# Performance work log

Hardware: AMD Instinct MI355X
Metric: run time of the kernel (lower is better)

## Reference

```python
import jax, jax.numpy as jnp
import numpy as np

B, N, D, K = 16, 65536, 24, 512
ATTRACTION_WEIGHT = 1.0
REPULSION_WEIGHT = 1.5
MARGIN_WEIGHT = 5.0
THRESHOLD = 0.5
MARGIN = 0.2
TAU = 0.7


def setup_inputs() -> dict:
    key = jax.random.key(0)
    k1, k2, k3 = jax.random.split(key, 3)
    beta = jax.random.normal(k1, (B, N, 1), jnp.float32)
    embed = jax.random.normal(k2, (B, N, D), jnp.float32)
    # First K hits of each event are the condensation points (one per instance),
    # remaining hits get a random instance id in [0, K).
    rand_sid = jax.random.randint(k3, (B, N - K), 0, K, jnp.int32)
    cp_sid = jnp.broadcast_to(jnp.arange(K, dtype=jnp.int32), (B, K))
    slice_id = jnp.concatenate([cp_sid, rand_sid], axis=1)
    is_cp = jnp.concatenate(
        [jnp.ones((B, K), jnp.int32), jnp.zeros((B, N - K), jnp.int32)], axis=1)
    return {"beta": beta, "embed": embed, "slice_id": slice_id, "is_cp": is_cp}


def _per_batch(beta_b, emb_b, sid, cp):
    # beta_b: [N], emb_b: [N, D], sid: [N] int, cp: [N] int
    n = beta_b.shape[0]
    f32 = beta_b.dtype
    cp_mask = cp == 1
    pos_count = cp_mask.sum()
    neg_count = n - pos_count

    seg_cnt = jax.ops.segment_sum(jnp.ones((n,), f32), sid, num_segments=K)
    inst_present = seg_cnt > 0
    cp_per_inst = jax.ops.segment_sum(cp_mask.astype(f32), sid, num_segments=K)
    valid_inst = inst_present & (cp_per_inst == 1)  # inst_cp.sum() == 1

    # --- grouped softmax CE over each instance (temperature TAU) ---
    logits = jnp.clip(beta_b, -20.0, 20.0) / TAU
    seg_max = jax.ops.segment_max(logits, sid, num_segments=K)
    safe_max = jnp.where(inst_present, seg_max, 0.0)
    ex = jnp.exp(logits - safe_max[sid])
    denom = jax.ops.segment_sum(ex, sid, num_segments=K)
    cp_logit = jax.ops.segment_sum(jnp.where(cp_mask, logits, 0.0), sid,
                                   num_segments=K)  # exactly one cp when valid
    p_cp = jnp.exp(cp_logit - safe_max) / jnp.maximum(denom, 1e-30)
    loss_inst = -jnp.log(p_cp + 1e-9)
    slice_count = valid_inst.sum()
    beta_slice_ce = jnp.where(valid_inst, loss_inst, 0.0).sum() / jnp.maximum(slice_count, 1)

    # --- margin loss on sigmoid(beta) ---
    beta_prob = jax.nn.sigmoid(jnp.clip(beta_b, -20.0, 20.0))
    pos_m = jnp.where(cp_mask, jax.nn.relu(THRESHOLD + MARGIN - beta_prob), 0.0).sum() \
        / jnp.maximum(pos_count, 1)
    neg_m = jnp.where(cp_mask, 0.0, jax.nn.relu(beta_prob - (THRESHOLD - MARGIN))).sum() \
        / jnp.maximum(neg_count, 1)
    beta_loss = beta_slice_ce + MARGIN_WEIGHT * (pos_m + neg_m)

    # --- attraction: hits pulled to first CP of their instance ---
    idx = jnp.arange(n, dtype=jnp.int32)
    first_cp = jax.ops.segment_min(jnp.where(cp_mask, idx, n), sid, num_segments=K)
    has_cp = (first_cp < n) & inst_present
    cp_emb = emb_b[jnp.minimum(first_cp, n - 1)]  # [K, D]
    d2 = jnp.minimum(((emb_b - cp_emb[sid]) ** 2).sum(-1), 50.0)
    d2_mean = jax.ops.segment_sum(d2, sid, num_segments=K) / jnp.maximum(seg_cnt, 1.0)
    attraction = ATTRACTION_WEIGHT * jnp.where(has_cp, d2_mean, 0.0).sum()

    # --- repulsion: pairwise exp(-d2) between CP embeddings (incl. diagonal) ---
    m = has_cp.astype(f32)
    mcount = m.sum()
    sq = (cp_emb ** 2).sum(-1)
    pd2 = sq[:, None] + sq[None, :] - 2.0 * (cp_emb @ cp_emb.T)
    pd2 = jnp.clip(pd2, 0.0, 50.0)
    rep = (jnp.exp(-pd2) * (m[:, None] * m[None, :])).sum() / jnp.maximum(mcount * mcount, 1.0)
    repulsion = jnp.where(mcount > 1, REPULSION_WEIGHT * rep, 0.0)

    valid = (pos_count >= 1) & (neg_count >= 1) & (slice_count > 0)
    total = beta_loss + attraction + repulsion
    return total, beta_loss, attraction, repulsion, valid


def reference(beta, embed, slice_id, is_cp):
    beta = jnp.nan_to_num(jnp.squeeze(beta, -1), nan=0.0, posinf=0.0, neginf=0.0)
    embed = jnp.nan_to_num(embed, nan=0.0, posinf=0.0, neginf=0.0)
    total, bl, al, rl, valid = jax.vmap(_per_batch)(beta, embed, slice_id, is_cp)
    v = valid.astype(beta.dtype)
    count = v.sum()
    safe = jnp.maximum(count, 1.0)
    ok = count > 0
    final = jnp.where(ok, (total * v).sum() / safe, 0.0)
    beta_log = jnp.where(ok, (bl * v).sum() / safe, 0.0)
    attr_log = jnp.where(ok, (al * v).sum() / safe, 0.0)
    repl_log = jnp.where(ok, (rl * v).sum() / safe, 0.0)
    return final, beta_log, attr_log, repl_log
```

## Files before the change

### kernel.cpp

```cpp
#include <hip/hip_runtime.h>
#include <math.h>

#define BB 16
#define NN 65536
#define DD 24
#define KK 512
#define CH 64
#define HPB (NN / CH)
#define TPB 256
#define RPB 8

__device__ __forceinline__ float fixnum(float v) {
  return __builtin_isfinite(v) ? v : 0.0f;
}

__device__ __forceinline__ float blockReduceSum(float v, float* sbuf) {
  __syncthreads();
  #pragma unroll
  for (int off = 32; off > 0; off >>= 1) v += __shfl_down(v, off, 64);
  int wid = threadIdx.x >> 6, lane = threadIdx.x & 63;
  if (lane == 0) sbuf[wid] = v;
  __syncthreads();
  return sbuf[0] + sbuf[1] + sbuf[2] + sbuf[3];
}

__global__ __launch_bounds__(TPB) void k1_seg(
    const float* __restrict__ beta, const int* __restrict__ sid,
    const int* __restrict__ iscp,
    float* __restrict__ cnt_p, float* __restrict__ den_p,
    float* __restrict__ cpc_p, float* __restrict__ cpl_p,
    int* __restrict__ first_p, float* __restrict__ marg_p)
{
  __shared__ float s_cnt[KK], s_den[KK], s_cpc[KK], s_cpl[KK];
  __shared__ int   s_first[KK];
  __shared__ float sred[4];
  int b = blockIdx.x >> 6, c = blockIdx.x & 63, t = threadIdx.x;
  for (int k = t; k < KK; k += TPB) {
    s_cnt[k] = 0.f; s_den[k] = 0.f; s_cpc[k] = 0.f; s_cpl[k] = 0.f; s_first[k] = NN;
  }
  __syncthreads();
  int h0 = c * HPB + t * 4;
  size_t g0 = (size_t)b * NN + h0;
  float4 bv = *(const float4*)(beta + g0);
  int4   sv = *(const int4*)(sid + g0);
  int4   cv = *(const int4*)(iscp + g0);
  float pm = 0.f, nm = 0.f;
  float bs[4] = {bv.x, bv.y, bv.z, bv.w};
  int   ss[4] = {sv.x, sv.y, sv.z, sv.w};
  int   cs[4] = {cv.x, cv.y, cv.z, cv.w};
  #pragma unroll
  for (int j = 0; j < 4; ++j) {
    float bc = fminf(fmaxf(fixnum(bs[j]), -20.f), 20.f);
    float logit = bc * (1.0f / 0.7f);
    int s = ss[j];
    atomicAdd(&s_cnt[s], 1.0f);
    atomicAdd(&s_den[s], __expf(logit));
    float prob = 1.0f / (1.0f + __expf(-bc));
    if (cs[j] == 1) {
      atomicAdd(&s_cpc[s], 1.0f);
      atomicAdd(&s_cpl[s], logit);
      atomicMin(&s_first[s], h0 + j);
      pm += fmaxf(0.7f - prob, 0.f);
    } else {
      nm += fmaxf(prob - 0.3f, 0.f);
    }
  }
  float pms = blockReduceSum(pm, sred);
  float nms = blockReduceSum(nm, sred);
  if (t == 0) { marg_p[2 * blockIdx.x] = pms; marg_p[2 * blockIdx.x + 1] = nms; }
  __syncthreads();
  size_t base = ((size_t)b * CH + c) * KK;
  for (int k = t; k < KK; k += TPB) {
    cnt_p[base + k] = s_cnt[k]; den_p[base + k] = s_den[k];
    cpc_p[base + k] = s_cpc[k]; cpl_p[base + k] = s_cpl[k];
    first_p[base + k] = s_first[k];
  }
}

__global__ __launch_bounds__(TPB) void k2_fin(
    const float* __restrict__ embed,
    const float* __restrict__ cnt_p, const float* __restrict__ den_p,
    const float* __restrict__ cpc_p, const float* __restrict__ cpl_p,
    const int* __restrict__ first_p,
    float* __restrict__ seg_cnt, float* __restrict__ loss_v,
    float* __restrict__ valid_f, float* __restrict__ has_cp_f,
    float* __restrict__ cpc_tot, float* __restrict__ cp_emb,
    float* __restrict__ d2_acc, float* __restrict__ rep_acc)
{
  int idx = blockIdx.x * TPB + threadIdx.x;
  int b = idx >> 9, k = idx & (KK - 1);
  float cnt = 0.f, den = 0.f, cpc = 0.f, cpl = 0.f;
  int fc = NN;
  #pragma unroll 8
  for (int c = 0; c < CH; ++c) {
    size_t base = ((size_t)b * CH + c) * KK + k;
    cnt += cnt_p[base]; den += den_p[base];
    cpc += cpc_p[base]; cpl += cpl_p[base];
    fc = min(fc, first_p[base]);
  }
  bool present = cnt > 0.f;
  bool vinst = present && (cpc == 1.0f);
  float p = __expf(cpl) / fmaxf(den, 1e-30f);
  seg_cnt[idx] = cnt;
  cpc_tot[idx] = cpc;
  loss_v[idx] = vinst ? -__logf(p + 1e-9f) : 0.f;
  valid_f[idx] = vinst ? 1.f : 0.f;
  has_cp_f[idx] = ((fc < NN) && present) ? 1.f : 0.f;
  d2_acc[idx] = 0.f;
  if (idx < BB) rep_acc[idx] = 0.f;
  int row = fc < NN ? fc : NN - 1;
  const float4* src = (const float4*)(embed + ((size_t)b * NN + row) * DD);
  float4* dst = (float4*)(cp_emb + (size_t)idx * DD);
  #pragma unroll
  for (int q = 0; q < DD / 4; ++q) {
    float4 v = src[q];
    v.x = fixnum(v.x); v.y = fixnum(v.y); v.z = fixnum(v.z); v.w = fixnum(v.w);
    dst[q] = v;
  }
}

__global__ __launch_bounds__(TPB) void k3_attr_rep(
    const float* __restrict__ embed, const int* __restrict__ sid,
    const float* __restrict__ cp_emb, const float* __restrict__ has_cp_f,
    float* __restrict__ d2_acc, float* __restrict__ rep_acc)
{
  __shared__ __align__(16) float s_ce[KK * DD];
  __shared__ float s_tile[64 * 25];
  __shared__ float s_d2[KK];
  int b = blockIdx.x >> 6, c = blockIdx.x & 63, t = threadIdx.x;

  const float4* ceg = (const float4*)(cp_emb + (size_t)b * KK * DD);
  float4* ces = (float4*)s_ce;
  #pragma unroll
  for (int i = 0; i < (KK * DD / 4) / TPB; ++i)
    ces[t + i * TPB] = ceg[t + i * TPB];
  for (int k = t; k < KK; k += TPB) s_d2[k] = 0.f;

  int hl = t >> 2, q = t & 3, d0 = q * 6;
  int rbase = hl * 25 + d0;
  int wI[3];
  #pragma unroll
  for (int j = 0; j < 3; ++j) {
    int f = 2 * (t + j * TPB);
    int h = f / 24;
    wI[j] = h * 25 + (f - h * 24);
  }

  size_t hit0 = (size_t)b * NN + (size_t)c * HPB;
  const float2* eb2 = (const float2*)(embed + hit0 * DD);
  const int* sidb = sid + hit0;

  float2 r[3];
  #pragma unroll
  for (int j = 0; j < 3; ++j) r[j] = eb2[t + j * TPB];
  __syncthreads();

  for (int tile = 0; tile < 16; ++tile) {
    #pragma unroll
    for (int j = 0; j < 3; ++j) {
      s_tile[wI[j]]     = fixnum(r[j].x);
      s_tile[wI[j] + 1] = fixnum(r[j].y);
    }
    __syncthreads();
    if (tile < 15) {
      const float2* nb = eb2 + (size_t)(tile + 1) * (64 * DD / 2);
      #pragma unroll
      for (int j = 0; j < 3; ++j) r[j] = nb[t + j * TPB];
    }
    int s = sidb[tile * 64 + hl];
    int cbase = s * DD + d0;
    float d2 = 0.f;
    #pragma unroll
    for (int d = 0; d < 6; ++d) {
      float x = s_tile[rbase + d] - s_ce[cbase + d];
      d2 += x * x;
    }
    d2 += __shfl_xor(d2, 1, 64);
    d2 += __shfl_xor(d2, 2, 64);
    if (q == 0) atomicAdd(&s_d2[s], fminf(d2, 50.f));
    __syncthreads();
  }

  for (int k = t; k < KK; k += TPB)
    atomicAdd(&d2_acc[b * KK + k], s_d2[k]);

  int j0 = t, j1 = t + TPB;
  float cj0[DD], cj1[DD];
  const float4* cj0p = (const float4*)(s_ce + j0 * DD);
  const float4* cj1p = (const float4*)(s_ce + j1 * DD);
  #pragma unroll
  for (int qq = 0; qq < DD / 4; ++qq) {
    float4 a = cj0p[qq], bq = cj1p[qq];
    cj0[qq*4] = a.x; cj0[qq*4+1] = a.y; cj0[qq*4+2] = a.z; cj0[qq*4+3] = a.w;
    cj1[qq*4] = bq.x; cj1[qq*4+1] = bq.y; cj1[qq*4+2] = bq.z; cj1[qq*4+3] = bq.w;
  }
  float m0 = has_cp_f[b * KK + j0], m1 = has_cp_f[b * KK + j1];
  float acc = 0.f;
  #pragma unroll
  for (int ri = 0; ri < RPB; ++ri) {
    int i = c * RPB + ri;
    float mi = has_cp_f[b * KK + i];
    float d20 = 0.f, d21 = 0.f;
    #pragma unroll
    for (int d = 0; d < DD; ++d) {
      float ci = s_ce[i * DD + d];
      float x0 = ci - cj0[d]; d20 += x0 * x0;
      float x1 = ci - cj1[d]; d21 += x1 * x1;
    }
    acc += mi * (m0 * __expf(-fminf(d20, 50.f)) + m1 * __expf(-fminf(d21, 50.f)));
  }
  float tot = blockReduceSum(acc, s_d2);
  if (t == 0) atomicAdd(&rep_acc[b], tot);
}

__global__ __launch_bounds__(1024) void k4_final(
    const float* __restrict__ d2_acc, const float* __restrict__ seg_cnt,
    const float* __restrict__ loss_v, const float* __restrict__ valid_f,
    const float* __restrict__ cpc_tot, const float* __restrict__ has_cp_f,
    const float* __restrict__ marg_p, const float* __restrict__ rep_acc,
    float* __restrict__ out)
{
  __shared__ float s_b[BB][5];
  int w = threadIdx.x >> 6, l = threadIdx.x & 63;
  int b = w;
  float attr = 0.f, ce = 0.f, vcnt = 0.f, pcnt = 0.f, mcnt = 0.f;
  #pragma unroll
  for (int k = l; k < KK; k += 64) {
    int idx = b * KK + k;
    float hc = has_cp_f[idx];
    attr += hc * (d2_acc[idx] / fmaxf(seg_cnt[idx], 1.f));
    ce   += loss_v[idx];
    vcnt += valid_f[idx];
    pcnt += cpc_tot[idx];
    mcnt += hc;
  }
  float pm = marg_p[(b * CH + l) * 2];
  float nm = marg_p[(b * CH + l) * 2 + 1];
  #pragma unroll
  for (int off = 32; off > 0; off >>= 1) {
    attr += __shfl_down(attr, off, 64);
    ce   += __shfl_down(ce, off, 64);
    vcnt += __shfl_down(vcnt, off, 64);
    pcnt += __shfl_down(pcnt, off, 64);
    mcnt += __shfl_down(mcnt, off, 64);
    pm   += __shfl_down(pm, off, 64);
    nm   += __shfl_down(nm, off, 64);
  }
  if (l == 0) {
    float pos = pcnt, neg = (float)NN - pos;
    float slice_ce = ce / fmaxf(vcnt, 1.f);
    float beta_loss = slice_ce + 5.0f * (pm / fmaxf(pos, 1.f) + nm / fmaxf(neg, 1.f));
    float rep = rep_acc[b] / fmaxf(mcnt * mcnt, 1.f);
    float repulsion = (mcnt > 1.f) ? 1.5f * rep : 0.f;
    float v = (pos >= 1.f && neg >= 1.f && vcnt > 0.f) ? 1.f : 0.f;
    s_b[w][0] = (beta_loss + attr + repulsion) * v;
    s_b[w][1] = beta_loss * v;
    s_b[w][2] = attr * v;
    s_b[w][3] = repulsion * v;
    s_b[w][4] = v;
  }
  __syncthreads();
  if (threadIdx.x == 0) {
    float s0 = 0.f, s1 = 0.f, s2 = 0.f, s3 = 0.f, cv = 0.f;
    #pragma unroll
    for (int i = 0; i < BB; ++i) {
      s0 += s_b[i][0]; s1 += s_b[i][1]; s2 += s_b[i][2]; s3 += s_b[i][3]; cv += s_b[i][4];
    }
    float safe = fmaxf(cv, 1.f);
    bool ok = cv > 0.f;
    out[0] = ok ? s0 / safe : 0.f;
    out[1] = ok ? s1 / safe : 0.f;
    out[2] = ok ? s2 / safe : 0.f;
    out[3] = ok ? s3 / safe : 0.f;
  }
}

extern "C" void kernel_launch(void* const* d_in, const int* in_sizes, int n_in,
                              void* d_out, int out_size, void* d_ws, size_t ws_size,
                              hipStream_t stream) {
  (void)in_sizes; (void)n_in; (void)out_size; (void)ws_size;
  const float* beta  = (const float*)d_in[0];
  const float* embed = (const float*)d_in[1];
  const int*   sid   = (const int*)d_in[2];
  const int*   iscp  = (const int*)d_in[3];
  float* out = (float*)d_out;
  char* ws = (char*)d_ws;

  size_t off = 0;
  auto alloc = [&](size_t bytes) {
    size_t o = off; off += (bytes + 255) & ~(size_t)255; return o;
  };
  const size_t BCK = (size_t)BB * CH * KK * 4;
  const size_t BKf = (size_t)BB * KK * 4;
  size_t o_cnt_p  = alloc(BCK);
  size_t o_den_p  = alloc(BCK);
  size_t o_cpc_p  = alloc(BCK);
  size_t o_cpl_p  = alloc(BCK);
  size_t o_first  = alloc(BCK);
  size_t o_marg   = alloc((size_t)BB * CH * 2 * 4);
  size_t o_segc   = alloc(BKf);
  size_t o_lossv  = alloc(BKf);
  size_t o_validf = alloc(BKf);
  size_t o_hascp  = alloc(BKf);
  size_t o_cpct   = alloc(BKf);
  size_t o_d2     = alloc(BKf);
  size_t o_cpe    = alloc((size_t)BB * KK * DD * 4);
  size_t o_rep    = alloc((size_t)BB * 4);

  k1_seg<<<BB * CH, TPB, 0, stream>>>(beta, sid, iscp,
      (float*)(ws + o_cnt_p), (float*)(ws + o_den_p),
      (float*)(ws + o_cpc_p), (float*)(ws + o_cpl_p),
      (int*)(ws + o_first), (float*)(ws + o_marg));

  k2_fin<<<(BB * KK) / TPB, TPB, 0, stream>>>(embed,
      (const float*)(ws + o_cnt_p), (const float*)(ws + o_den_p),
      (const float*)(ws + o_cpc_p), (const float*)(ws + o_cpl_p),
      (const int*)(ws + o_first),
      (float*)(ws + o_segc), (float*)(ws + o_lossv), (float*)(ws + o_validf),
      (float*)(ws + o_hascp), (float*)(ws + o_cpct), (float*)(ws + o_cpe),
      (float*)(ws + o_d2), (float*)(ws + o_rep));

  k3_attr_rep<<<BB * CH, TPB, 0, stream>>>(embed, sid,
      (const float*)(ws + o_cpe), (const float*)(ws + o_hascp),
      (float*)(ws + o_d2), (float*)(ws + o_rep));

  k4_final<<<1, 1024, 0, stream>>>((const float*)(ws + o_d2),
      (const float*)(ws + o_segc), (const float*)(ws + o_lossv),
      (const float*)(ws + o_validf), (const float*)(ws + o_cpct),
      (const float*)(ws + o_hascp), (const float*)(ws + o_marg),
      (const float*)(ws + o_rep), out);
}
```

Baseline: 206.1 us.

## Fuse four kernels into one cooperative persistent kernel with grid syncs

Replaces the four-launch pipeline with a single cooperative kernel of 256 blocks × 512 threads that runs segment reduction, per-instance finalize, attraction/repulsion and the final reduction, separated by grid.sync(). It also changes the work split: 16 chunks per batch instead of 64, each block handling twice as many hits per tile, and 32 repulsion rows per block. The aim is to remove launch gaps and inter-kernel tail effects. In exchange it uses fewer, larger blocks, relies on grid-wide barriers, and runs the finalize stage on only 16 blocks, with the old path kept as a fallback if the cooperative launch fails.

```diff
diff --git a/kernel.cpp b/kernel.cpp
--- a/kernel.cpp
+++ b/kernel.cpp
@@ -1,10 +1,17 @@
 #include <hip/hip_runtime.h>
+#include <hip/hip_cooperative_groups.h>
 #include <math.h>
+
+namespace cg = cooperative_groups;
 
 #define BB 16
 #define NN 65536
 #define DD 24
 #define KK 512
+#define FBLK 256
+#define FTPB 512
+#define FCPB 16
+#define FHPB (NN / FCPB)
 #define CH 64
 #define HPB (NN / CH)
 #define TPB 256
@@ -14,14 +21,274 @@
   return __builtin_isfinite(v) ? v : 0.0f;
 }
 
-__device__ __forceinline__ float blockReduceSum(float v, float* sbuf) {
+__device__ __forceinline__ float blockReduceSum8(float v, float* sbuf) {
   __syncthreads();
   #pragma unroll
   for (int off = 32; off > 0; off >>= 1) v += __shfl_down(v, off, 64);
   int wid = threadIdx.x >> 6, lane = threadIdx.x & 63;
   if (lane == 0) sbuf[wid] = v;
   __syncthreads();
+  float s = 0.f;
+  #pragma unroll
+  for (int i = 0; i < 8; ++i) s += sbuf[i];
+  return s;
+}
+
+__device__ __forceinline__ float blockReduceSum(float v, float* sbuf) {
+  __syncthreads();
+  #pragma unroll
+  for (int off = 32; off > 0; off >>= 1) v += __shfl_down(v, off, 64);
+  int wid = threadIdx.x >> 6, lane = threadIdx.x & 63;
+  if (lane == 0) sbuf[wid] = v;
+  __syncthreads();
   return sbuf[0] + sbuf[1] + sbuf[2] + sbuf[3];
+}
+
+__global__ __launch_bounds__(FTPB, 2) void kfused(
+    const float* __restrict__ beta, const float* __restrict__ embed,
+    const int* __restrict__ sid, const int* __restrict__ iscp,
+    float* __restrict__ cnt_p, float* __restrict__ den_p,
+    float* __restrict__ cpc_p, float* __restrict__ cpl_p,
+    int* __restrict__ first_p, float* __restrict__ marg_p,
+    float* __restrict__ seg_cnt, float* __restrict__ loss_v,
+    float* __restrict__ valid_f, float* __restrict__ has_cp_f,
+    float* __restrict__ cpc_tot, float* __restrict__ cp_emb,
+    float* __restrict__ d2_acc, float* __restrict__ rep_acc,
+    float* __restrict__ out)
+{
+  __shared__ __align__(16) float s_ce[KK * DD];
+  __shared__ float s_tile[128 * 25];
+  __shared__ float s_d2[KK];
+  __shared__ float sred[8];
+  __shared__ float s_b[BB][5];
+
+  cg::grid_group grid = cg::this_grid();
+  int blk = blockIdx.x, t = threadIdx.x;
+  int b = blk >> 4, qc = blk & 15;
+
+  {
+    float* s_cnt = s_ce;
+    float* s_den = s_ce + KK;
+    float* s_cpc = s_ce + 2 * KK;
+    float* s_cpl = s_ce + 3 * KK;
+    int*   s_first = (int*)(s_ce + 4 * KK);
+    if (t < KK) {
+      s_cnt[t] = 0.f; s_den[t] = 0.f; s_cpc[t] = 0.f; s_cpl[t] = 0.f;
+      s_first[t] = NN;
+    }
+    __syncthreads();
+    int h0 = qc * FHPB + t * 8;
+    size_t g0 = (size_t)b * NN + h0;
+    float4 bv0 = *(const float4*)(beta + g0);
+    float4 bv1 = *(const float4*)(beta + g0 + 4);
+    int4   sv0 = *(const int4*)(sid + g0);
+    int4   sv1 = *(const int4*)(sid + g0 + 4);
+    int4   cv0 = *(const int4*)(iscp + g0);
+    int4   cv1 = *(const int4*)(iscp + g0 + 4);
+    float bs[8] = {bv0.x, bv0.y, bv0.z, bv0.w, bv1.x, bv1.y, bv1.z, bv1.w};
+    int   ss[8] = {sv0.x, sv0.y, sv0.z, sv0.w, sv1.x, sv1.y, sv1.z, sv1.w};
+    int   cs[8] = {cv0.x, cv0.y, cv0.z, cv0.w, cv1.x, cv1.y, cv1.z, cv1.w};
+    float pm = 0.f, nm = 0.f;
+    #pragma unroll
+    for (int j = 0; j < 8; ++j) {
+      float bc = fminf(fmaxf(fixnum(bs[j]), -20.f), 20.f);
+      float logit = bc * (1.0f / 0.7f);
+      int s = ss[j];
+      atomicAdd(&s_cnt[s], 1.0f);
+      atomicAdd(&s_den[s], __expf(logit));
+      float prob = 1.0f / (1.0f + __expf(-bc));
+      if (cs[j] == 1) {
+        atomicAdd(&s_cpc[s], 1.0f);
+        atomicAdd(&s_cpl[s], logit);
+        atomicMin(&s_first[s], h0 + j);
+        pm += fmaxf(0.7f - prob, 0.f);
+      } else {
+        nm += fmaxf(prob - 0.3f, 0.f);
+      }
+    }
+    float pms = blockReduceSum8(pm, sred);
+    float nms = blockReduceSum8(nm, sred);
+    if (t == 0) { marg_p[2 * blk] = pms; marg_p[2 * blk + 1] = nms; }
+    __syncthreads();
+    size_t base = (size_t)blk * KK;
+    if (t < KK) {
+      cnt_p[base + t] = s_cnt[t]; den_p[base + t] = s_den[t];
+      cpc_p[base + t] = s_cpc[t]; cpl_p[base + t] = s_cpl[t];
+      first_p[base + t] = s_first[t];
+    }
+  }
+  grid.sync();
+
+  if (blk < BB) {
+    int bb = blk, k = t;
+    float cnt = 0.f, den = 0.f, cpc = 0.f, cpl = 0.f;
+    int fc = NN;
+    #pragma unroll 4
+    for (int c = 0; c < FCPB; ++c) {
+      size_t base = ((size_t)bb * FCPB + c) * KK + k;
+      cnt += cnt_p[base]; den += den_p[base];
+      cpc += cpc_p[base]; cpl += cpl_p[base];
+      fc = min(fc, first_p[base]);
+    }
+    int idx = bb * KK + k;
+    bool present = cnt > 0.f;
+    bool vinst = present && (cpc == 1.0f);
+    float p = __expf(cpl) / fmaxf(den, 1e-30f);
+    seg_cnt[idx] = cnt;
+    cpc_tot[idx] = cpc;
+    loss_v[idx] = vinst ? -__logf(p + 1e-9f) : 0.f;
+    valid_f[idx] = vinst ? 1.f : 0.f;
+    has_cp_f[idx] = ((fc < NN) && present) ? 1.f : 0.f;
+    d2_acc[idx] = 0.f;
+    if (blk == 0 && t < BB) rep_acc[t] = 0.f;
+    int row = fc < NN ? fc : NN - 1;
+    const float4* src = (const float4*)(embed + ((size_t)bb * NN + row) * DD);
+    float4* dst = (float4*)(cp_emb + (size_t)idx * DD);
+    #pragma unroll
+    for (int q = 0; q < DD / 4; ++q) {
+      float4 v = src[q];
+      v.x = fixnum(v.x); v.y = fixnum(v.y); v.z = fixnum(v.z); v.w = fixnum(v.w);
+      dst[q] = v;
+    }
+  }
+  grid.sync();
+
+  {
+    const float4* ceg = (const float4*)(cp_emb + (size_t)b * KK * DD);
+    float4* ces = (float4*)s_ce;
+    #pragma unroll
+    for (int i = 0; i < (KK * DD / 4) / FTPB; ++i)
+      ces[t + i * FTPB] = ceg[t + i * FTPB];
+    if (t < KK) s_d2[t] = 0.f;
+
+    int hl = t >> 2, q = t & 3, d0 = q * 6;
+    int rbase = hl * 25 + d0;
+    int wI[3];
+    #pragma unroll
+    for (int j = 0; j < 3; ++j) {
+      int f = 2 * (t + j * FTPB);
+      int h = f / 24;
+      wI[j] = h * 25 + (f - h * 24);
+    }
+    size_t hit0 = (size_t)b * NN + (size_t)qc * FHPB;
+    const float2* eb2 = (const float2*)(embed + hit0 * DD);
+    const int* sidb = sid + hit0;
+
+    float2 r[3];
+    #pragma unroll
+    for (int j = 0; j < 3; ++j) r[j] = eb2[t + j * FTPB];
+    __syncthreads();
+
+    for (int tile = 0; tile < 32; ++tile) {
+      #pragma unroll
+      for (int j = 0; j < 3; ++j) {
+        s_tile[wI[j]]     = fixnum(r[j].x);
+        s_tile[wI[j] + 1] = fixnum(r[j].y);
+      }
+      __syncthreads();
+      if (tile < 31) {
+        const float2* nb = eb2 + (size_t)(tile + 1) * (128 * DD / 2);
+        #pragma unroll
+        for (int j = 0; j < 3; ++j) r[j] = nb[t + j * FTPB];
+      }
+      int s = sidb[tile * 128 + hl];
+      int cbase = s * DD + d0;
+      float d2 = 0.f;
+      #pragma unroll
+      for (int d = 0; d < 6; ++d) {
+        float x = s_tile[rbase + d] - s_ce[cbase + d];
+        d2 += x * x;
+      }
+      d2 += __shfl_xor(d2, 1, 64);
+      d2 += __shfl_xor(d2, 2, 64);
+      if (q == 0) atomicAdd(&s_d2[s], fminf(d2, 50.f));
+      __syncthreads();
+    }
+    if (t < KK) atomicAdd(&d2_acc[b * KK + t], s_d2[t]);
+
+    int j0 = t;
+    float cj[DD];
+    const float4* cjp = (const float4*)(s_ce + j0 * DD);
+    #pragma unroll
+    for (int qq = 0; qq < DD / 4; ++qq) {
+      float4 a = cjp[qq];
+      cj[qq*4] = a.x; cj[qq*4+1] = a.y; cj[qq*4+2] = a.z; cj[qq*4+3] = a.w;
+    }
+    float m0 = has_cp_f[b * KK + j0];
+    float acc = 0.f;
+    #pragma unroll 4
+    for (int ri = 0; ri < 32; ++ri) {
+      int i2 = qc * 32 + ri;
+      float mi = has_cp_f[b * KK + i2];
+      float d2r = 0.f;
+      #pragma unroll
+      for (int d = 0; d < DD; ++d) {
+        float x = s_ce[i2 * DD + d] - cj[d];
+        d2r += x * x;
+      }
+      acc += mi * m0 * __expf(-fminf(d2r, 50.f));
+    }
+    float tot = blockReduceSum8(acc, sred);
+    if (t == 0) atomicAdd(&rep_acc[b], tot);
+  }
+  grid.sync();
+
+  if (blk == 0) {
+    int w = t >> 6, l = t & 63;
+    for (int bb = w; bb < BB; bb += 8) {
+      float attr = 0.f, ce = 0.f, vcnt = 0.f, pcnt = 0.f, mcnt = 0.f;
+      #pragma unroll
+      for (int k = l; k < KK; k += 64) {
+        int idx = bb * KK + k;
+        float hc = has_cp_f[idx];
+        attr += hc * (d2_acc[idx] / fmaxf(seg_cnt[idx], 1.f));
+        ce   += loss_v[idx];
+        vcnt += valid_f[idx];
+        pcnt += cpc_tot[idx];
+        mcnt += hc;
+      }
+      float pm = (l < FCPB) ? marg_p[2 * (bb * FCPB + l)] : 0.f;
+      float nm = (l < FCPB) ? marg_p[2 * (bb * FCPB + l) + 1] : 0.f;
+      #pragma unroll
+      for (int off = 32; off > 0; off >>= 1) {
+        attr += __shfl_down(attr, off, 64);
+        ce   += __shfl_down(ce, off, 64);
+        vcnt += __shfl_down(vcnt, off, 64);
+        pcnt += __shfl_down(pcnt, off, 64);
+        mcnt += __shfl_down(mcnt, off, 64);
+        pm   += __shfl_down(pm, off, 64);
+        nm   += __shfl_down(nm, off, 64);
+      }
+      if (l == 0) {
+        float pos = pcnt, neg = (float)NN - pos;
+        float slice_ce = ce / fmaxf(vcnt, 1.f);
+        float beta_loss = slice_ce + 5.0f * (pm / fmaxf(pos, 1.f) + nm / fmaxf(neg, 1.f));
+        float rep = rep_acc[bb] / fmaxf(mcnt * mcnt, 1.f);
+        float repulsion = (mcnt > 1.f) ? 1.5f * rep : 0.f;
+        float v = (pos >= 1.f && neg >= 1.f && vcnt > 0.f) ? 1.f : 0.f;
+        s_b[bb][0] = (beta_loss + attr + repulsion) * v;
+        s_b[bb][1] = beta_loss * v;
+        s_b[bb][2] = attr * v;
+        s_b[bb][3] = repulsion * v;
+        s_b[bb][4] = v;
+      }
+    }
+    __syncthreads();
+    if (t == 0) {
+      float s0 = 0.f, s1 = 0.f, s2 = 0.f, s3 = 0.f, cv = 0.f;
+      #pragma unroll
+      for (int i = 0; i < BB; ++i) {
+        s0 += s_b[i][0]; s1 += s_b[i][1]; s2 += s_b[i][2]; s3 += s_b[i][3];
+        cv += s_b[i][4];
+      }
+      float safe = fmaxf(cv, 1.f);
+      bool ok = cv > 0.f;
+      out[0] = ok ? s0 / safe : 0.f;
+      out[1] = ok ? s1 / safe : 0.f;
+      out[2] = ok ? s2 / safe : 0.f;
+      out[3] = ok ? s3 / safe : 0.f;
+    }
+  }
 }
 
 __global__ __launch_bounds__(TPB) void k1_seg(
@@ -128,14 +395,12 @@
   __shared__ float s_tile[64 * 25];
   __shared__ float s_d2[KK];
   int b = blockIdx.x >> 6, c = blockIdx.x & 63, t = threadIdx.x;
-
   const float4* ceg = (const float4*)(cp_emb + (size_t)b * KK * DD);
   float4* ces = (float4*)s_ce;
   #pragma unroll
   for (int i = 0; i < (KK * DD / 4) / TPB; ++i)
     ces[t + i * TPB] = ceg[t + i * TPB];
   for (int k = t; k < KK; k += TPB) s_d2[k] = 0.f;
-
   int hl = t >> 2, q = t & 3, d0 = q * 6;
   int rbase = hl * 25 + d0;
   int wI[3];
@@ -145,16 +410,13 @@
     int h = f / 24;
     wI[j] = h * 25 + (f - h * 24);
   }
-
   size_t hit0 = (size_t)b * NN + (size_t)c * HPB;
   const float2* eb2 = (const float2*)(embed + hit0 * DD);
   const int* sidb = sid + hit0;
-
   float2 r[3];
   #pragma unroll
   for (int j = 0; j < 3; ++j) r[j] = eb2[t + j * TPB];
   __syncthreads();
-
   for (int tile = 0; tile < 16; ++tile) {
     #pragma unroll
     for (int j = 0; j < 3; ++j) {
@@ -180,10 +442,8 @@
     if (q == 0) atomicAdd(&s_d2[s], fminf(d2, 50.f));
     __syncthreads();
   }
-
   for (int k = t; k < KK; k += TPB)
     atomicAdd(&d2_acc[b * KK + k], s_d2[k]);
-
   int j0 = t, j1 = t + TPB;
   float cj0[DD], cj1[DD];
   const float4* cj0p = (const float4*)(s_ce + j0 * DD);
@@ -307,26 +567,40 @@
   size_t o_cpe    = alloc((size_t)BB * KK * DD * 4);
   size_t o_rep    = alloc((size_t)BB * 4);
 
-  k1_seg<<<BB * CH, TPB, 0, stream>>>(beta, sid, iscp,
-      (float*)(ws + o_cnt_p), (float*)(ws + o_den_p),
-      (float*)(ws + o_cpc_p), (float*)(ws + o_cpl_p),
-      (int*)(ws + o_first), (float*)(ws + o_marg));
-
-  k2_fin<<<(BB * KK) / TPB, TPB, 0, stream>>>(embed,
-      (const float*)(ws + o_cnt_p), (const float*)(ws + o_den_p),
-      (const float*)(ws + o_cpc_p), (const float*)(ws + o_cpl_p),
-      (const int*)(ws + o_first),
-      (float*)(ws + o_segc), (float*)(ws + o_lossv), (float*)(ws + o_validf),
-      (float*)(ws + o_hascp), (float*)(ws + o_cpct), (float*)(ws + o_cpe),
-      (float*)(ws + o_d2), (float*)(ws + o_rep));
-
-  k3_attr_rep<<<BB * CH, TPB, 0, stream>>>(embed, sid,
-      (const float*)(ws + o_cpe), (const float*)(ws + o_hascp),
-      (float*)(ws + o_d2), (float*)(ws + o_rep));
-
-  k4_final<<<1, 1024, 0, stream>>>((const float*)(ws + o_d2),
-      (const float*)(ws + o_segc), (const float*)(ws + o_lossv),
-      (const float*)(ws + o_validf), (const float*)(ws + o_cpct),
-      (const float*)(ws + o_hascp), (const float*)(ws + o_marg),
-      (const float*)(ws + o_rep), out);
-}
+  float* p_cnt  = (float*)(ws + o_cnt_p);
+  float* p_den  = (float*)(ws + o_den_p);
+  float* p_cpc  = (float*)(ws + o_cpc_p);
+  float* p_cpl  = (float*)(ws + o_cpl_p);
+  int*   p_fst  = (int*)(ws + o_first);
+  float* p_marg = (float*)(ws + o_marg);
+  float* p_segc = (float*)(ws + o_segc);
+  float* p_lossv= (float*)(ws + o_lossv);
+  float* p_vldf = (float*)(ws + o_validf);
+  float* p_hcp  = (float*)(ws + o_hascp);
+  float* p_cpct = (float*)(ws + o_cpct);
+  float* p_d2   = (float*)(ws + o_d2);
+  float* p_cpe  = (float*)(ws + o_cpe);
+  float* p_rep  = (float*)(ws + o_rep);
+
+  void* args[] = {
+    (void*)&beta, (void*)&embed, (void*)&sid, (void*)&iscp,
+    (void*)&p_cnt, (void*)&p_den, (void*)&p_cpc, (void*)&p_cpl,
+    (void*)&p_fst, (void*)&p_marg, (void*)&p_segc, (void*)&p_lossv,
+    (void*)&p_vldf, (void*)&p_hcp, (void*)&p_cpct, (void*)&p_cpe,
+    (void*)&p_d2, (void*)&p_rep, (void*)&out
+  };
+  hipError_t err = hipLaunchCooperativeKernel(
+      (const void*)kfused, dim3(FBLK), dim3(FTPB), args, 0, stream);
+
+  if (err != hipSuccess) {
+    k1_seg<<<BB * CH, TPB, 0, stream>>>(beta, sid, iscp,
+        p_cnt, p_den, p_cpc, p_cpl, p_fst, p_marg);
+    k2_fin<<<(BB * KK) / TPB, TPB, 0, stream>>>(embed,
+        p_cnt, p_den, p_cpc, p_cpl, p_fst,
+        p_segc, p_lossv, p_vldf, p_hcp, p_cpct, p_cpe, p_d2, p_rep);
+    k3_attr_rep<<<BB * CH, TPB, 0, stream>>>(embed, sid,
+        p_cpe, p_hcp, p_d2, p_rep);
+    k4_final<<<1, 1024, 0, stream>>>(p_d2, p_segc, p_lossv, p_vldf,
+        p_cpct, p_hcp, p_marg, p_rep, out);
+  }
+}
```

New measurement: 287.7 us. 39.6% more time.

## Replace per-chunk partial buffers with global atomics and drop finalize kernel

Applied to the files above, without the earlier changes.

k1 now merges its shared-memory segment partials straight into per-batch global arrays with atomics, skipping zero entries, instead of writing per-chunk partial arrays. This removes the k2 reduction kernel and its cp_emb gather. k3 no longer stages all condensation-point embeddings in LDS; it reads them from global memory through the first-index table, which shrinks LDS use and may raise occupancy. k4 computes the per-instance CE terms itself. The change adds two memsets and global atomic traffic, plus scattered global reads in the attraction and repulsion loops, and it changes has_cp (no longer requires present, though the two are equivalent here).

```diff
diff --git a/kernel.cpp b/kernel.cpp
--- a/kernel.cpp
+++ b/kernel.cpp
@@ -9,6 +9,7 @@
 #define HPB (NN / CH)
 #define TPB 256
 #define RPB 8
+#define FIRST_INIT 0x7F7F7F7F
 
 __device__ __forceinline__ float fixnum(float v) {
   return __builtin_isfinite(v) ? v : 0.0f;
@@ -27,9 +28,9 @@
 __global__ __launch_bounds__(TPB) void k1_seg(
     const float* __restrict__ beta, const int* __restrict__ sid,
     const int* __restrict__ iscp,
-    float* __restrict__ cnt_p, float* __restrict__ den_p,
-    float* __restrict__ cpc_p, float* __restrict__ cpl_p,
-    int* __restrict__ first_p, float* __restrict__ marg_p)
+    float* __restrict__ cnt_g, float* __restrict__ den_g,
+    float* __restrict__ cpc_g, float* __restrict__ cpl_g,
+    int* __restrict__ first_g, float* __restrict__ marg_g)
 {
   __shared__ float s_cnt[KK], s_den[KK], s_cpc[KK], s_cpl[KK];
   __shared__ int   s_first[KK];
@@ -67,74 +68,40 @@
   }
   float pms = blockReduceSum(pm, sred);
   float nms = blockReduceSum(nm, sred);
-  if (t == 0) { marg_p[2 * blockIdx.x] = pms; marg_p[2 * blockIdx.x + 1] = nms; }
-  __syncthreads();
-  size_t base = ((size_t)b * CH + c) * KK;
+  if (t == 0) {
+    if (pms != 0.f) atomicAdd(&marg_g[2 * b], pms);
+    if (nms != 0.f) atomicAdd(&marg_g[2 * b + 1], nms);
+  }
+  __syncthreads();
+  int base = b * KK;
   for (int k = t; k < KK; k += TPB) {
-    cnt_p[base + k] = s_cnt[k]; den_p[base + k] = s_den[k];
-    cpc_p[base + k] = s_cpc[k]; cpl_p[base + k] = s_cpl[k];
-    first_p[base + k] = s_first[k];
-  }
-}
-
-__global__ __launch_bounds__(TPB) void k2_fin(
-    const float* __restrict__ embed,
-    const float* __restrict__ cnt_p, const float* __restrict__ den_p,
-    const float* __restrict__ cpc_p, const float* __restrict__ cpl_p,
-    const int* __restrict__ first_p,
-    float* __restrict__ seg_cnt, float* __restrict__ loss_v,
-    float* __restrict__ valid_f, float* __restrict__ has_cp_f,
-    float* __restrict__ cpc_tot, float* __restrict__ cp_emb,
+    if (s_cnt[k] != 0.f) {
+      atomicAdd(&cnt_g[base + k], s_cnt[k]);
+      atomicAdd(&den_g[base + k], s_den[k]);
+    }
+    if (s_cpc[k] != 0.f) {
+      atomicAdd(&cpc_g[base + k], s_cpc[k]);
+      atomicAdd(&cpl_g[base + k], s_cpl[k]);
+    }
+    if (s_first[k] < NN) atomicMin(&first_g[base + k], s_first[k]);
+  }
+}
+
+__global__ __launch_bounds__(TPB) void k3_attr_rep(
+    const float* __restrict__ embed, const int* __restrict__ sid,
+    const int* __restrict__ first_g,
     float* __restrict__ d2_acc, float* __restrict__ rep_acc)
 {
-  int idx = blockIdx.x * TPB + threadIdx.x;
-  int b = idx >> 9, k = idx & (KK - 1);
-  float cnt = 0.f, den = 0.f, cpc = 0.f, cpl = 0.f;
-  int fc = NN;
-  #pragma unroll 8
-  for (int c = 0; c < CH; ++c) {
-    size_t base = ((size_t)b * CH + c) * KK + k;
-    cnt += cnt_p[base]; den += den_p[base];
-    cpc += cpc_p[base]; cpl += cpl_p[base];
-    fc = min(fc, first_p[base]);
-  }
-  bool present = cnt > 0.f;
-  bool vinst = present && (cpc == 1.0f);
-  float p = __expf(cpl) / fmaxf(den, 1e-30f);
-  seg_cnt[idx] = cnt;
-  cpc_tot[idx] = cpc;
-  loss_v[idx] = vinst ? -__logf(p + 1e-9f) : 0.f;
-  valid_f[idx] = vinst ? 1.f : 0.f;
-  has_cp_f[idx] = ((fc < NN) && present) ? 1.f : 0.f;
-  d2_acc[idx] = 0.f;
-  if (idx < BB) rep_acc[idx] = 0.f;
-  int row = fc < NN ? fc : NN - 1;
-  const float4* src = (const float4*)(embed + ((size_t)b * NN + row) * DD);
-  float4* dst = (float4*)(cp_emb + (size_t)idx * DD);
-  #pragma unroll
-  for (int q = 0; q < DD / 4; ++q) {
-    float4 v = src[q];
-    v.x = fixnum(v.x); v.y = fixnum(v.y); v.z = fixnum(v.z); v.w = fixnum(v.w);
-    dst[q] = v;
-  }
-}
-
-__global__ __launch_bounds__(TPB) void k3_attr_rep(
-    const float* __restrict__ embed, const int* __restrict__ sid,
-    const float* __restrict__ cp_emb, const float* __restrict__ has_cp_f,
-    float* __restrict__ d2_acc, float* __restrict__ rep_acc)
-{
-  __shared__ __align__(16) float s_ce[KK * DD];
   __shared__ float s_tile[64 * 25];
   __shared__ float s_d2[KK];
+  __shared__ int   s_first[KK];
+  __shared__ float sred[4];
   int b = blockIdx.x >> 6, c = blockIdx.x & 63, t = threadIdx.x;
 
-  const float4* ceg = (const float4*)(cp_emb + (size_t)b * KK * DD);
-  float4* ces = (float4*)s_ce;
-  #pragma unroll
-  for (int i = 0; i < (KK * DD / 4) / TPB; ++i)
-    ces[t + i * TPB] = ceg[t + i * TPB];
-  for (int k = t; k < KK; k += TPB) s_d2[k] = 0.f;
+  for (int k = t; k < KK; k += TPB) {
+    s_first[k] = first_g[b * KK + k];
+    s_d2[k] = 0.f;
+  }
 
   int hl = t >> 2, q = t & 3, d0 = q * 6;
   int rbase = hl * 25 + d0;
@@ -147,6 +114,7 @@
   }
 
   size_t hit0 = (size_t)b * NN + (size_t)c * HPB;
+  const float* embB = embed + (size_t)b * NN * DD;
   const float2* eb2 = (const float2*)(embed + hit0 * DD);
   const int* sidb = sid + hit0;
 
@@ -168,11 +136,16 @@
       for (int j = 0; j < 3; ++j) r[j] = nb[t + j * TPB];
     }
     int s = sidb[tile * 64 + hl];
-    int cbase = s * DD + d0;
+    int fs = s_first[s];
+    int row = fs < NN ? fs : 0;
+    const float2* cep = (const float2*)(embB + (size_t)row * DD + d0);
+    float2 c0 = cep[0], c1 = cep[1], c2 = cep[2];
+    float ce[6] = {fixnum(c0.x), fixnum(c0.y), fixnum(c1.x),
+                   fixnum(c1.y), fixnum(c2.x), fixnum(c2.y)};
     float d2 = 0.f;
     #pragma unroll
     for (int d = 0; d < 6; ++d) {
-      float x = s_tile[rbase + d] - s_ce[cbase + d];
+      float x = s_tile[rbase + d] - ce[d];
       d2 += x * x;
     }
     d2 += __shfl_xor(d2, 1, 64);
@@ -185,39 +158,45 @@
     atomicAdd(&d2_acc[b * KK + k], s_d2[k]);
 
   int j0 = t, j1 = t + TPB;
+  int f0 = s_first[j0], f1 = s_first[j1];
+  float m0 = f0 < NN ? 1.f : 0.f, m1 = f1 < NN ? 1.f : 0.f;
+  int r0 = f0 < NN ? f0 : 0, r1 = f1 < NN ? f1 : 0;
   float cj0[DD], cj1[DD];
-  const float4* cj0p = (const float4*)(s_ce + j0 * DD);
-  const float4* cj1p = (const float4*)(s_ce + j1 * DD);
+  const float4* cj0p = (const float4*)(embB + (size_t)r0 * DD);
+  const float4* cj1p = (const float4*)(embB + (size_t)r1 * DD);
   #pragma unroll
   for (int qq = 0; qq < DD / 4; ++qq) {
     float4 a = cj0p[qq], bq = cj1p[qq];
-    cj0[qq*4] = a.x; cj0[qq*4+1] = a.y; cj0[qq*4+2] = a.z; cj0[qq*4+3] = a.w;
-    cj1[qq*4] = bq.x; cj1[qq*4+1] = bq.y; cj1[qq*4+2] = bq.z; cj1[qq*4+3] = bq.w;
-  }
-  float m0 = has_cp_f[b * KK + j0], m1 = has_cp_f[b * KK + j1];
+    cj0[qq*4]   = fixnum(a.x);  cj0[qq*4+1] = fixnum(a.y);
+    cj0[qq*4+2] = fixnum(a.z);  cj0[qq*4+3] = fixnum(a.w);
+    cj1[qq*4]   = fixnum(bq.x); cj1[qq*4+1] = fixnum(bq.y);
+    cj1[qq*4+2] = fixnum(bq.z); cj1[qq*4+3] = fixnum(bq.w);
+  }
   float acc = 0.f;
   #pragma unroll
   for (int ri = 0; ri < RPB; ++ri) {
     int i = c * RPB + ri;
-    float mi = has_cp_f[b * KK + i];
+    int fi = s_first[i];
+    float mi = fi < NN ? 1.f : 0.f;
+    const float* rowp = embB + (size_t)(fi < NN ? fi : 0) * DD;
     float d20 = 0.f, d21 = 0.f;
     #pragma unroll
     for (int d = 0; d < DD; ++d) {
-      float ci = s_ce[i * DD + d];
+      float ci = fixnum(rowp[d]);
       float x0 = ci - cj0[d]; d20 += x0 * x0;
       float x1 = ci - cj1[d]; d21 += x1 * x1;
     }
     acc += mi * (m0 * __expf(-fminf(d20, 50.f)) + m1 * __expf(-fminf(d21, 50.f)));
   }
-  float tot = blockReduceSum(acc, s_d2);
+  float tot = blockReduceSum(acc, sred);
   if (t == 0) atomicAdd(&rep_acc[b], tot);
 }
 
 __global__ __launch_bounds__(1024) void k4_final(
-    const float* __restrict__ d2_acc, const float* __restrict__ seg_cnt,
-    const float* __restrict__ loss_v, const float* __restrict__ valid_f,
-    const float* __restrict__ cpc_tot, const float* __restrict__ has_cp_f,
-    const float* __restrict__ marg_p, const float* __restrict__ rep_acc,
+    const float* __restrict__ cnt_g, const float* __restrict__ den_g,
+    const float* __restrict__ cpc_g, const float* __restrict__ cpl_g,
+    const int* __restrict__ first_g, const float* __restrict__ d2_acc,
+    const float* __restrict__ marg_g, const float* __restrict__ rep_acc,
     float* __restrict__ out)
 {
   __shared__ float s_b[BB][5];
@@ -227,15 +206,20 @@
   #pragma unroll
   for (int k = l; k < KK; k += 64) {
     int idx = b * KK + k;
-    float hc = has_cp_f[idx];
-    attr += hc * (d2_acc[idx] / fmaxf(seg_cnt[idx], 1.f));
-    ce   += loss_v[idx];
-    vcnt += valid_f[idx];
-    pcnt += cpc_tot[idx];
+    float cnt = cnt_g[idx], den = den_g[idx];
+    float cpc = cpc_g[idx], cpl = cpl_g[idx];
+    int   fc  = first_g[idx];
+    float d2  = d2_acc[idx];
+    bool present = cnt > 0.f;
+    bool vinst = present && (cpc == 1.0f);
+    float p = __expf(cpl) / fmaxf(den, 1e-30f);
+    float hc = (fc < NN) ? 1.f : 0.f;
+    ce   += vinst ? -__logf(p + 1e-9f) : 0.f;
+    attr += hc * (d2 / fmaxf(cnt, 1.f));
+    vcnt += vinst ? 1.f : 0.f;
+    pcnt += cpc;
     mcnt += hc;
   }
-  float pm = marg_p[(b * CH + l) * 2];
-  float nm = marg_p[(b * CH + l) * 2 + 1];
   #pragma unroll
   for (int off = 32; off > 0; off >>= 1) {
     attr += __shfl_down(attr, off, 64);
@@ -243,10 +227,9 @@
     vcnt += __shfl_down(vcnt, off, 64);
     pcnt += __shfl_down(pcnt, off, 64);
     mcnt += __shfl_down(mcnt, off, 64);
-    pm   += __shfl_down(pm, off, 64);
-    nm   += __shfl_down(nm, off, 64);
   }
   if (l == 0) {
+    float pm = marg_g[2 * b], nm = marg_g[2 * b + 1];
     float pos = pcnt, neg = (float)NN - pos;
     float slice_ce = ce / fmaxf(vcnt, 1.f);
     float beta_loss = slice_ce + 5.0f * (pm / fmaxf(pos, 1.f) + nm / fmaxf(neg, 1.f));
@@ -290,43 +273,35 @@
   auto alloc = [&](size_t bytes) {
     size_t o = off; off += (bytes + 255) & ~(size_t)255; return o;
   };
-  const size_t BCK = (size_t)BB * CH * KK * 4;
   const size_t BKf = (size_t)BB * KK * 4;
-  size_t o_cnt_p  = alloc(BCK);
-  size_t o_den_p  = alloc(BCK);
-  size_t o_cpc_p  = alloc(BCK);
-  size_t o_cpl_p  = alloc(BCK);
-  size_t o_first  = alloc(BCK);
-  size_t o_marg   = alloc((size_t)BB * CH * 2 * 4);
-  size_t o_segc   = alloc(BKf);
-  size_t o_lossv  = alloc(BKf);
-  size_t o_validf = alloc(BKf);
-  size_t o_hascp  = alloc(BKf);
-  size_t o_cpct   = alloc(BKf);
-  size_t o_d2     = alloc(BKf);
-  size_t o_cpe    = alloc((size_t)BB * KK * DD * 4);
-  size_t o_rep    = alloc((size_t)BB * 4);
+  size_t o_zero  = alloc(0);
+  size_t o_cnt   = alloc(BKf);
+  size_t o_den   = alloc(BKf);
+  size_t o_cpc   = alloc(BKf);
+  size_t o_cpl   = alloc(BKf);
+  size_t o_d2    = alloc(BKf);
+  size_t o_marg  = alloc((size_t)BB * 2 * 4);
+  size_t o_rep   = alloc((size_t)BB * 4);
+  size_t zbytes  = off - o_zero;
+  size_t o_first = alloc(BKf);
+
+  float* p_cnt  = (float*)(ws + o_cnt);
+  float* p_den  = (float*)(ws + o_den);
+  float* p_cpc  = (float*)(ws + o_cpc);
+  float* p_cpl  = (float*)(ws + o_cpl);
+  float* p_d2   = (float*)(ws + o_d2);
+  float* p_marg = (float*)(ws + o_marg);
+  float* p_rep  = (float*)(ws + o_rep);
+  int*   p_fst  = (int*)(ws + o_first);
+
+  hipMemsetAsync(ws + o_zero, 0, zbytes, stream);
+  hipMemsetAsync(ws + o_first, 0x7F, BKf, stream);
 
   k1_seg<<<BB * CH, TPB, 0, stream>>>(beta, sid, iscp,
-      (float*)(ws + o_cnt_p), (float*)(ws + o_den_p),
-      (float*)(ws + o_cpc_p), (float*)(ws + o_cpl_p),
-      (int*)(ws + o_first), (float*)(ws + o_marg));
-
-  k2_fin<<<(BB * KK) / TPB, TPB, 0, stream>>>(embed,
-      (const float*)(ws + o_cnt_p), (const float*)(ws + o_den_p),
-      (const float*)(ws + o_cpc_p), (const float*)(ws + o_cpl_p),
-      (const int*)(ws + o_first),
-      (float*)(ws + o_segc), (float*)(ws + o_lossv), (float*)(ws + o_validf),
-      (float*)(ws + o_hascp), (float*)(ws + o_cpct), (float*)(ws + o_cpe),
-      (float*)(ws + o_d2), (float*)(ws + o_rep));
-
-  k3_attr_rep<<<BB * CH, TPB, 0, stream>>>(embed, sid,
-      (const float*)(ws + o_cpe), (const float*)(ws + o_hascp),
-      (float*)(ws + o_d2), (float*)(ws + o_rep));
-
-  k4_final<<<1, 1024, 0, stream>>>((const float*)(ws + o_d2),
-      (const float*)(ws + o_segc), (const float*)(ws + o_lossv),
-      (const float*)(ws + o_validf), (const float*)(ws + o_cpct),
-      (const float*)(ws + o_hascp), (const float*)(ws + o_marg),
-      (const float*)(ws + o_rep), out);
-}
+      p_cnt, p_den, p_cpc, p_cpl, p_fst, p_marg);
+
+  k3_attr_rep<<<BB * CH, TPB, 0, stream>>>(embed, sid, p_fst, p_d2, p_rep);
+
+  k4_final<<<1, 1024, 0, stream>>>(p_cnt, p_den, p_cpc, p_cpl,
+      p_fst, p_d2, p_marg, p_rep, out);
+}
```

Measured after the change: 210.5 us. 2.1% more time.
